# Performance work log

Hardware: AMD Instinct MI355X
Metric: run time of the kernel (lower is better)

The kernel has to match this reference:

```python
import jax, jax.numpy as jnp
import numpy as np

N_NODES, EMB, HID, HEADS, E = 50000, 128, 64, 3, 800000


def setup_inputs() -> dict:
    key = jax.random.key(0)
    ks = jax.random.split(key, 12)
    HC = HEADS * HID
    return {
        "edge_index": jax.random.randint(ks[0], (2, E), 0, N_NODES),
        "edge_attr": jax.random.uniform(ks[1], (E, 1), dtype=jnp.float32),
        "path_emb": jax.random.normal(ks[2], (N_NODES, EMB), dtype=jnp.float32) * (2.0 / EMB) ** 0.5,
        "sim_w": jnp.ones((1,), dtype=jnp.float32),
        "Wl": jax.random.normal(ks[3], (HC, EMB), dtype=jnp.float32) / np.sqrt(EMB),
        "bl": jnp.zeros((HC,), dtype=jnp.float32),
        "Wr": jax.random.normal(ks[4], (HC, EMB), dtype=jnp.float32) / np.sqrt(EMB),
        "br": jnp.zeros((HC,), dtype=jnp.float32),
        "We": jax.random.normal(ks[5], (HC, 1), dtype=jnp.float32),
        "att": jax.random.normal(ks[6], (1, HEADS, HID), dtype=jnp.float32) / np.sqrt(HID),
        "bias_gnn": jnp.zeros((HID,), dtype=jnp.float32),
        "Wout": jax.random.normal(ks[7], (1, HID), dtype=jnp.float32) / np.sqrt(HID),
        "bout": jnp.zeros((1,), dtype=jnp.float32),
    }


def reference(edge_index, edge_attr, path_emb, sim_w, Wl, bl, Wr, br, We, att, bias_gnn, Wout, bout):
    # SimFusionModule: softmax-weighted combination over sim channels -> [E, 1]
    w = jax.nn.softmax(sim_w, axis=0)
    fused = (edge_attr * w).sum(axis=1, keepdims=True)  # [E,1]

    # GATv2Conv (concat=False, no self loops, edge_dim=1)
    xl = (path_emb @ Wl.T + bl).reshape(-1, HEADS, HID)  # source transform [N,H,C]
    xr = (path_emb @ Wr.T + br).reshape(-1, HEADS, HID)  # target transform [N,H,C]
    src, dst = edge_index[0], edge_index[1]
    xj = xl[src]                                          # [E,H,C] gathered source
    xi = xr[dst]                                          # [E,H,C] gathered target
    ef = (fused @ We.T).reshape(-1, HEADS, HID)           # [E,H,C] edge features
    m = xj + xi + ef
    a = (jax.nn.leaky_relu(m, 0.2) * att).sum(-1)         # [E,H] attention logits

    # segment softmax over incoming edges of each destination node
    amax = jax.ops.segment_max(a, dst, num_segments=N_NODES)
    aexp = jnp.exp(a - amax[dst])
    asum = jax.ops.segment_sum(aexp, dst, num_segments=N_NODES)
    alpha = aexp / asum[dst]                              # [E,H]

    out = jax.ops.segment_sum(alpha[:, :, None] * xj, dst, num_segments=N_NODES)  # [N,H,C]
    out = out.mean(axis=1) + bias_gnn                     # concat=False -> head mean, + bias

    scores = (out @ Wout.T + bout).squeeze()              # [N]
    return jax.nn.softmax(scores, axis=0)
```

## Files before the change

### kernel.cpp

```cpp
#include <hip/hip_runtime.h>
#include <cfloat>
#include <cmath>

#define NHEADS 3
#define HIDC   64
#define HCC    192
#define EMBC   128
#define WCOLS  384
#define CAP    1280
#define SCH    4096

typedef unsigned short bhalf;
typedef __fp16 half_t;
typedef __attribute__((ext_vector_type(2))) __fp16 h2;
typedef __attribute__((ext_vector_type(8))) short bf16x8;
typedef __attribute__((ext_vector_type(4))) float f32x4;

__device__ __forceinline__ unsigned f2bf(float f) {
  unsigned u = __float_as_uint(f);
  return (u + 0x7FFFu + ((u >> 16) & 1u)) >> 16;
}
__device__ __forceinline__ unsigned h2bits(h2 v) {
  union { h2 h; unsigned u; } cv; cv.h = v; return cv.u;
}

__global__ __launch_bounds__(256) void prep_kernel(
    const float* __restrict__ Wl, const float* __restrict__ Wr,
    const float* __restrict__ bl, const float* __restrict__ br,
    const float* __restrict__ Wout, const float* __restrict__ We,
    const float* __restrict__ att,
    bhalf* __restrict__ Wb, float* __restrict__ vh, float* __restrict__ bfl,
    unsigned* __restrict__ weh, unsigned* __restrict__ atth,
    float* __restrict__ ch, unsigned* __restrict__ cur,
    float* __restrict__ sumexp, int NB)
{
  const int BASE = WCOLS * EMBC;
  int gt = blockIdx.x * 256 + threadIdx.x;
  if (gt < BASE) {
    int c = gt >> 7, k = gt & 127;
    float v = (c < HCC) ? Wl[c * EMBC + k] : Wr[(c - HCC) * EMBC + k];
    Wb[gt] = (bhalf)f2bf(v);
  } else if (gt < BASE + 384) {
    int i = gt - BASE;
    int h = i >> 7, k = i & 127;
    float s = 0.f;
    for (int c = 0; c < HIDC; ++c)
      s += Wout[c] * Wl[(h * HIDC + c) * EMBC + k];
    vh[i] = s;
  } else if (gt < BASE + 768) {
    int c = gt - BASE - 384;
    bfl[c] = (c < HCC) ? bl[c] : br[c - HCC];
  } else if (gt < BASE + 864) {
    int i = gt - BASE - 768;
    weh[i] = h2bits(__builtin_amdgcn_cvt_pkrtz(We[2 * i], We[2 * i + 1]));
  } else if (gt < BASE + 960) {
    int i = gt - BASE - 864;
    atth[i] = h2bits(__builtin_amdgcn_cvt_pkrtz(att[2 * i], att[2 * i + 1]));
  } else if (gt < BASE + 963) {
    int h = gt - BASE - 960;
    float s = 0.f;
    for (int c = 0; c < HIDC; ++c) s += bl[h * HIDC + c] * Wout[c];
    ch[h] = s;
  } else if (gt < BASE + 963 + NB) {
    int b = gt - BASE - 963;
    cur[b * 16] = (unsigned)(b * CAP);
  } else if (gt == BASE + 963 + NB) {
    *sumexp = 0.f;
  }
}

__global__ __launch_bounds__(256, 4) void gemmscatter_kernel(
    const float* __restrict__ pe, const bhalf* __restrict__ Wb,
    const float* __restrict__ bfl, const float* __restrict__ vh,
    const float* __restrict__ ch,
    half_t* __restrict__ xlh, half_t* __restrict__ xrh,
    float* __restrict__ pj, int N,
    const int* __restrict__ ei, const float* __restrict__ ea,
    uint2* __restrict__ eb, unsigned* __restrict__ cur, int E, int NB2)
{
  __shared__ union {
    bhalf Ws[192 * 64];
    struct { unsigned lh[800]; unsigned lbase[800]; } s;
  } sm;
  const int tid = threadIdx.x;

  if ((int)blockIdx.x < NB2) {
    const int w    = tid >> 6;
    const int lane = tid & 63;
    const int m    = lane & 15;
    const int q    = lane >> 4;
    const int nb   = blockIdx.x >> 1;
    const int half = blockIdx.x & 1;
    const int node = nb * 64 + w * 16 + m;
    const size_t prow = (size_t)(node < N ? node : N - 1) * EMBC;

    bf16x8 pfrag[4];
    float pjp[3] = {0.f, 0.f, 0.f};
    #pragma unroll
    for (int kt = 0; kt < 4; ++kt) {
      const float* p = pe + prow + kt * 32 + q * 8;
      float4 x = *(const float4*)p;
      float4 y = *(const float4*)(p + 4);
      if (half == 0) {
        #pragma unroll
        for (int h = 0; h < 3; ++h) {
          const float* v = vh + h * EMBC + kt * 32 + q * 8;
          float4 va = *(const float4*)v;
          float4 vb = *(const float4*)(v + 4);
          pjp[h] += x.x*va.x + x.y*va.y + x.z*va.z + x.w*va.w
                  + y.x*vb.x + y.y*vb.y + y.z*vb.z + y.w*vb.w;
        }
      }
      union { bf16x8 v; unsigned u[4]; } uu;
      uu.u[0] = (__float_as_uint(x.x) >> 16) | (__float_as_uint(x.y) & 0xFFFF0000u);
      uu.u[1] = (__float_as_uint(x.z) >> 16) | (__float_as_uint(x.w) & 0xFFFF0000u);
      uu.u[2] = (__float_as_uint(y.x) >> 16) | (__float_as_uint(y.y) & 0xFFFF0000u);
      uu.u[3] = (__float_as_uint(y.z) >> 16) | (__float_as_uint(y.w) & 0xFFFF0000u);
      pfrag[kt] = uu.v;
    }

    f32x4 acc[12];
    #pragma unroll
    for (int t = 0; t < 12; ++t) acc[t] = (f32x4){0.f, 0.f, 0.f, 0.f};

    for (int kh = 0; kh < 2; ++kh) {
      __syncthreads();
      for (int f = tid; f < 192 * 8; f += 256) {
        int cc = f >> 3, s = f & 7;
        uint4 v = *(const uint4*)(Wb + (size_t)(half * HCC + cc) * EMBC + kh * 64 + s * 8);
        *(uint4*)(sm.Ws + cc * 64 + ((s ^ (cc & 7)) * 8)) = v;
      }
      __syncthreads();
      #pragma unroll
      for (int kt2 = 0; kt2 < 2; ++kt2) {
        #pragma unroll
        for (int t = 0; t < 12; ++t) {
          bf16x8 wf = *(const bf16x8*)(sm.Ws + (t * 16 + m) * 64 + (((kt2 << 2) + q) ^ (m & 7)) * 8);
          acc[t] = __builtin_amdgcn_mfma_f32_16x16x32_bf16(wf, pfrag[kh * 2 + kt2], acc[t], 0, 0, 0);
        }
      }
    }

    if (half == 0) {
      #pragma unroll
      for (int h = 0; h < 3; ++h) {
        pjp[h] += __shfl_xor(pjp[h], 16);
        pjp[h] += __shfl_xor(pjp[h], 32);
      }
      if (q == 0 && node < N) {
        pj[node * 3 + 0] = pjp[0] + ch[0];
        pj[node * 3 + 1] = pjp[1] + ch[1];
        pj[node * 3 + 2] = pjp[2] + ch[2];
      }
    }

    if (node < N) {
      half_t* xo = half ? xrh : xlh;
      #pragma unroll
      for (int t = 0; t < 12; ++t) {
        int col = t * 16 + q * 4;
        float4 b = *(const float4*)(bfl + half * HCC + col);
        h2 pa = __builtin_amdgcn_cvt_pkrtz(acc[t][0] + b.x, acc[t][1] + b.y);
        h2 pb = __builtin_amdgcn_cvt_pkrtz(acc[t][2] + b.z, acc[t][3] + b.w);
        uint2 st; st.x = h2bits(pa); st.y = h2bits(pb);
        *(uint2*)(xo + (size_t)node * HCC + col) = st;
      }
    }
  } else {
    const int base = (blockIdx.x - NB2) * SCH;
    for (int i = tid; i < 800; i += 256) sm.s.lh[i] = 0;
    __syncthreads();
    #pragma unroll 4
    for (int i = 0; i < SCH / 256; ++i) {
      int e = base + i * 256 + tid;
      if (e < E) atomicAdd(&sm.s.lh[ei[E + e] >> 6], 1u);
    }
    __syncthreads();
    for (int i = tid; i < 800; i += 256) {
      unsigned c = sm.s.lh[i];
      sm.s.lbase[i] = c ? atomicAdd(&cur[i * 16], c) : 0u;
      sm.s.lh[i] = 0;
    }
    __syncthreads();
    #pragma unroll 4
    for (int i = 0; i < SCH / 256; ++i) {
      int e = base + i * 256 + tid;
      if (e < E) {
        int src = ei[e], dst = ei[E + e];
        int bin = dst >> 6;
        unsigned slot = sm.s.lbase[bin] + atomicAdd(&sm.s.lh[bin], 1u);
        uint2 rec;
        rec.x = (unsigned)src | ((unsigned)dst << 16);
        rec.y = __float_as_uint(ea[e]);
        eb[slot] = rec;
      }
    }
  }
}

#define EPG 5
#define GPW 4
#define WCHUNK (EPG * GPW)
__global__ __launch_bounds__(512, 4) void edge_kernel(
    const uint2* __restrict__ eb,
    const half_t* __restrict__ xlh, const half_t* __restrict__ xrh,
    const float* __restrict__ pj, const unsigned* __restrict__ weh,
    const unsigned* __restrict__ atth, const unsigned* __restrict__ cur,
    float* __restrict__ sumexp, float* __restrict__ out, int N)
{
  __shared__ uint4 xrs[64][25];
  __shared__ float facc[64][8];
  const int tid  = threadIdx.x;
  const int w    = tid >> 6;
  const int lane = tid & 63;
  const int j = lane / 12;
  const int c = lane % 12;
  const bool act = lane < 60;
  const int b = blockIdx.x;
  const int n0 = b << 6;
  const int start = b * CAP;
  const int end   = (int)cur[b * 16];

  for (int i = tid; i < 64 * 24; i += 512) {
    int row = i / 24, sl = i % 24;
    int nn = n0 + row; if (nn >= N) nn = N - 1;
    xrs[row][sl] = *(const uint4*)(xrh + (size_t)nn * HCC + sl * 8);
  }
  if (tid < 512) ((float*)facc)[tid] = 0.f;

  union U8 { uint4 u[2]; h2 h[8]; };
  U8 we, at;
  we.u[0] = *(const uint4*)(weh + c * 8);
  we.u[1] = *(const uint4*)(weh + c * 8 + 4);
  at.u[0] = *(const uint4*)(atth + c * 8);
  at.u[1] = *(const uint4*)(atth + c * 8 + 4);
  const h2 c02 = {(__fp16)0.2f, (__fp16)0.2f};
  __syncthreads();

  const int wstart = start + w * WCHUNK;
  uint2 rec[GPW];
  #pragma unroll
  for (int g = 0; g < GPW; ++g) {
    int e = wstart + g * EPG + j;
    rec[g] = eb[e < end ? e : start];
  }

  for (int cb = wstart; cb < end; cb += 8 * WCHUNK) {
    int srcs[GPW], dsts[GPW]; float eavs[GPW];
    #pragma unroll
    for (int g = 0; g < GPW; ++g) {
      srcs[g] = (int)(rec[g].x & 0xFFFFu);
      dsts[g] = (int)(rec[g].x >> 16);
      eavs[g] = __uint_as_float(rec[g].y);
    }
    union U8x { uint4 u[2]; h2 h[8]; };
    U8x ul[GPW]; float pjv[GPW];
    #pragma unroll
    for (int g = 0; g < GPW; ++g) {
      const half_t* rp = xlh + (size_t)srcs[g] * HCC + c * 16;
      ul[g].u[0] = ((const uint4*)rp)[0];
      ul[g].u[1] = ((const uint4*)rp)[1];
    }
    #pragma unroll
    for (int g = 0; g < GPW; ++g)
      pjv[g] = pj[srcs[g] * 3 + (c >> 2)];

    int nxt = cb + 8 * WCHUNK;
    #pragma unroll
    for (int g = 0; g < GPW; ++g) {
      int e = nxt + g * EPG + j;
      rec[g] = eb[(e < end) ? e : start];
    }

    #pragma unroll
    for (int g = 0; g < GPW; ++g) {
      int ld = dsts[g] & 63;
      U8x ur;
      ur.u[0] = xrs[ld][c * 2];
      ur.u[1] = xrs[ld][c * 2 + 1];
      h2 eav2 = __builtin_amdgcn_cvt_pkrtz(eavs[g], eavs[g]);
      float sc = 0.f;
      #pragma unroll
      for (int i = 0; i < 8; ++i) {
        h2 m  = ul[g].h[i] + ur.h[i] + eav2 * we.h[i];
        h2 lr = __builtin_elementwise_max(m, m * c02);
        sc = __builtin_amdgcn_fdot2(lr, at.h[i], sc, false);
      }
      sc += __shfl_xor(sc, 1);
      sc += __shfl_xor(sc, 2);
      bool ve = act && (cb + g * EPG + j < end);
      if (ve && (c & 3) == 0) {
        int h = c >> 2;
        float ex = __expf(sc);
        atomicAdd(&facc[ld][h], ex);
        atomicAdd(&facc[ld][3 + h], ex * pjv[g]);
      }
    }
  }
  __syncthreads();

  if (tid < 64) {
    int n = n0 + tid;
    float e = 0.f;
    if (n < N) {
      float accs = 0.f;
      #pragma unroll
      for (int h = 0; h < 3; ++h) {
        float d = facc[tid][h];
        if (d > 0.f) accs += facc[tid][3 + h] / d;
      }
      e = expf(accs * (1.f / 3.f));
      out[n] = e;
    }
    #pragma unroll
    for (int o = 32; o; o >>= 1) e += __shfl_xor(e, o);
    if (tid == 0) atomicAdd(sumexp, e);
  }
}

__global__ __launch_bounds__(256) void norm_kernel(
    float* __restrict__ out, const float* __restrict__ sumexp, int N)
{
  int n = blockIdx.x * 256 + threadIdx.x;
  if (n < N) out[n] /= *sumexp;
}

extern "C" void kernel_launch(void* const* d_in, const int* in_sizes, int n_in,
                              void* d_out, int out_size, void* d_ws, size_t ws_size,
                              hipStream_t stream) {
  const int*   ei   = (const int*)  d_in[0];
  const float* ea   = (const float*)d_in[1];
  const float* pe   = (const float*)d_in[2];
  const float* Wl   = (const float*)d_in[4];
  const float* bl   = (const float*)d_in[5];
  const float* Wr   = (const float*)d_in[6];
  const float* br   = (const float*)d_in[7];
  const float* We   = (const float*)d_in[8];
  const float* att  = (const float*)d_in[9];
  const float* Wout = (const float*)d_in[11];

  const int E = in_sizes[0] / 2;
  const int N = in_sizes[2] / EMBC;
  const int NB = (N + 63) >> 6;
  float* out = (float*)d_out;

  float* ws       = (float*)d_ws;
  float* sumexp   = ws;
  unsigned* cur   = (unsigned*)(ws + 16);
  float* pj       = ws + 16 + (size_t)NB * 16;
  float* vh       = pj + (size_t)3 * N;
  float* bfl      = vh + 384;
  unsigned* weh   = (unsigned*)(bfl + 384);
  unsigned* atth  = weh + 96;
  float* ch       = (float*)(atth + 96);
  bhalf* Wb       = (bhalf*)(ch + 16);
  half_t* xlh     = (half_t*)(Wb + (size_t)WCOLS * EMBC);
  half_t* xrh     = xlh + (size_t)N * HCC;
  uint2* eb       = (uint2*)(xrh + (size_t)N * HCC);

  const int BASE = WCOLS * EMBC;
  const int NB2 = NB * 2;
  const int NSC = (E + SCH - 1) / SCH;
  prep_kernel<<<(BASE + 963 + NB + 1 + 255) / 256, 256, 0, stream>>>(
      Wl, Wr, bl, br, Wout, We, att, Wb, vh, bfl, weh, atth, ch,
      cur, sumexp, NB);
  gemmscatter_kernel<<<NB2 + NSC, 256, 0, stream>>>(
      pe, Wb, bfl, vh, ch, xlh, xrh, pj, N, ei, ea, eb, cur, E, NB2);
  edge_kernel<<<NB, 512, 0, stream>>>(eb, xlh, xrh, pj, weh, atth, cur,
                                      sumexp, out, N);
  norm_kernel<<<(N + 255) / 256, 256, 0, stream>>>(out, sumexp, N);
}
```

Before: 211.9 us.

## Store node features in fp8, split edge buckets across blocks, add finalize kernel

Node projections xl/xr are now stored as scaled fp8 (x16) rather than fp16, which halves the bytes per gathered row in the edge kernel. The per-destination xr is gathered straight from global memory instead of being staged in shared memory. Each bucket is split across two 256-thread blocks that write partial accumulators, and a new finalize kernel combines them. The pj projection is now computed from the GEMM outputs with Wout instead of a precomputed vh dot product, and the scatter blocks are ordered first. fp8 storage lowers precision and adds conversion work, and the extra kernel launch adds overhead.

```diff
diff --git a/kernel.cpp b/kernel.cpp
--- a/kernel.cpp
+++ b/kernel.cpp
@@ -9,12 +9,14 @@
 #define WCOLS  384
 #define CAP    1280
 #define SCH    4096
+#define SPLIT  2
 
 typedef unsigned short bhalf;
 typedef __fp16 half_t;
 typedef __attribute__((ext_vector_type(2))) __fp16 h2;
 typedef __attribute__((ext_vector_type(8))) short bf16x8;
 typedef __attribute__((ext_vector_type(4))) float f32x4;
+typedef __attribute__((ext_vector_type(2))) float f32x2;
 
 __device__ __forceinline__ unsigned f2bf(float f) {
   unsigned u = __float_as_uint(f);
@@ -27,12 +29,10 @@
 __global__ __launch_bounds__(256) void prep_kernel(
     const float* __restrict__ Wl, const float* __restrict__ Wr,
     const float* __restrict__ bl, const float* __restrict__ br,
-    const float* __restrict__ Wout, const float* __restrict__ We,
-    const float* __restrict__ att,
-    bhalf* __restrict__ Wb, float* __restrict__ vh, float* __restrict__ bfl,
+    const float* __restrict__ We, const float* __restrict__ att,
+    bhalf* __restrict__ Wb, float* __restrict__ bfl,
     unsigned* __restrict__ weh, unsigned* __restrict__ atth,
-    float* __restrict__ ch, unsigned* __restrict__ cur,
-    float* __restrict__ sumexp, int NB)
+    unsigned* __restrict__ cur, float* __restrict__ sumexp, int NB)
 {
   const int BASE = WCOLS * EMBC;
   int gt = blockIdx.x * 256 + threadIdx.x;
@@ -41,42 +41,30 @@
     float v = (c < HCC) ? Wl[c * EMBC + k] : Wr[(c - HCC) * EMBC + k];
     Wb[gt] = (bhalf)f2bf(v);
   } else if (gt < BASE + 384) {
-    int i = gt - BASE;
-    int h = i >> 7, k = i & 127;
-    float s = 0.f;
-    for (int c = 0; c < HIDC; ++c)
-      s += Wout[c] * Wl[(h * HIDC + c) * EMBC + k];
-    vh[i] = s;
-  } else if (gt < BASE + 768) {
-    int c = gt - BASE - 384;
+    int c = gt - BASE;
     bfl[c] = (c < HCC) ? bl[c] : br[c - HCC];
-  } else if (gt < BASE + 864) {
-    int i = gt - BASE - 768;
-    weh[i] = h2bits(__builtin_amdgcn_cvt_pkrtz(We[2 * i], We[2 * i + 1]));
-  } else if (gt < BASE + 960) {
-    int i = gt - BASE - 864;
-    atth[i] = h2bits(__builtin_amdgcn_cvt_pkrtz(att[2 * i], att[2 * i + 1]));
-  } else if (gt < BASE + 963) {
-    int h = gt - BASE - 960;
-    float s = 0.f;
-    for (int c = 0; c < HIDC; ++c) s += bl[h * HIDC + c] * Wout[c];
-    ch[h] = s;
-  } else if (gt < BASE + 963 + NB) {
-    int b = gt - BASE - 963;
+  } else if (gt < BASE + 480) {
+    int i = gt - BASE - 384;
+    weh[i] = h2bits(__builtin_amdgcn_cvt_pkrtz(16.f * We[2 * i], 16.f * We[2 * i + 1]));
+  } else if (gt < BASE + 576) {
+    int i = gt - BASE - 480;
+    atth[i] = h2bits(__builtin_amdgcn_cvt_pkrtz(att[2 * i] * (1.f / 16.f),
+                                                att[2 * i + 1] * (1.f / 16.f)));
+  } else if (gt < BASE + 576 + NB) {
+    int b = gt - BASE - 576;
     cur[b * 16] = (unsigned)(b * CAP);
-  } else if (gt == BASE + 963 + NB) {
+  } else if (gt == BASE + 576 + NB) {
     *sumexp = 0.f;
   }
 }
 
 __global__ __launch_bounds__(256, 4) void gemmscatter_kernel(
     const float* __restrict__ pe, const bhalf* __restrict__ Wb,
-    const float* __restrict__ bfl, const float* __restrict__ vh,
-    const float* __restrict__ ch,
-    half_t* __restrict__ xlh, half_t* __restrict__ xrh,
+    const float* __restrict__ bfl, const float* __restrict__ Wout,
+    unsigned char* __restrict__ xl8, unsigned char* __restrict__ xr8,
     float* __restrict__ pj, int N,
     const int* __restrict__ ei, const float* __restrict__ ea,
-    uint2* __restrict__ eb, unsigned* __restrict__ cur, int E, int NB2)
+    uint2* __restrict__ eb, unsigned* __restrict__ cur, int E, int NSC)
 {
   __shared__ union {
     bhalf Ws[192 * 64];
@@ -84,90 +72,8 @@
   } sm;
   const int tid = threadIdx.x;
 
-  if ((int)blockIdx.x < NB2) {
-    const int w    = tid >> 6;
-    const int lane = tid & 63;
-    const int m    = lane & 15;
-    const int q    = lane >> 4;
-    const int nb   = blockIdx.x >> 1;
-    const int half = blockIdx.x & 1;
-    const int node = nb * 64 + w * 16 + m;
-    const size_t prow = (size_t)(node < N ? node : N - 1) * EMBC;
-
-    bf16x8 pfrag[4];
-    float pjp[3] = {0.f, 0.f, 0.f};
-    #pragma unroll
-    for (int kt = 0; kt < 4; ++kt) {
-      const float* p = pe + prow + kt * 32 + q * 8;
-      float4 x = *(const float4*)p;
-      float4 y = *(const float4*)(p + 4);
-      if (half == 0) {
-        #pragma unroll
-        for (int h = 0; h < 3; ++h) {
-          const float* v = vh + h * EMBC + kt * 32 + q * 8;
-          float4 va = *(const float4*)v;
-          float4 vb = *(const float4*)(v + 4);
-          pjp[h] += x.x*va.x + x.y*va.y + x.z*va.z + x.w*va.w
-                  + y.x*vb.x + y.y*vb.y + y.z*vb.z + y.w*vb.w;
-        }
-      }
-      union { bf16x8 v; unsigned u[4]; } uu;
-      uu.u[0] = (__float_as_uint(x.x) >> 16) | (__float_as_uint(x.y) & 0xFFFF0000u);
-      uu.u[1] = (__float_as_uint(x.z) >> 16) | (__float_as_uint(x.w) & 0xFFFF0000u);
-      uu.u[2] = (__float_as_uint(y.x) >> 16) | (__float_as_uint(y.y) & 0xFFFF0000u);
-      uu.u[3] = (__float_as_uint(y.z) >> 16) | (__float_as_uint(y.w) & 0xFFFF0000u);
-      pfrag[kt] = uu.v;
-    }
-
-    f32x4 acc[12];
-    #pragma unroll
-    for (int t = 0; t < 12; ++t) acc[t] = (f32x4){0.f, 0.f, 0.f, 0.f};
-
-    for (int kh = 0; kh < 2; ++kh) {
-      __syncthreads();
-      for (int f = tid; f < 192 * 8; f += 256) {
-        int cc = f >> 3, s = f & 7;
-        uint4 v = *(const uint4*)(Wb + (size_t)(half * HCC + cc) * EMBC + kh * 64 + s * 8);
-        *(uint4*)(sm.Ws + cc * 64 + ((s ^ (cc & 7)) * 8)) = v;
-      }
-      __syncthreads();
-      #pragma unroll
-      for (int kt2 = 0; kt2 < 2; ++kt2) {
-        #pragma unroll
-        for (int t = 0; t < 12; ++t) {
-          bf16x8 wf = *(const bf16x8*)(sm.Ws + (t * 16 + m) * 64 + (((kt2 << 2) + q) ^ (m & 7)) * 8);
-          acc[t] = __builtin_amdgcn_mfma_f32_16x16x32_bf16(wf, pfrag[kh * 2 + kt2], acc[t], 0, 0, 0);
-        }
-      }
-    }
-
-    if (half == 0) {
-      #pragma unroll
-      for (int h = 0; h < 3; ++h) {
-        pjp[h] += __shfl_xor(pjp[h], 16);
-        pjp[h] += __shfl_xor(pjp[h], 32);
-      }
-      if (q == 0 && node < N) {
-        pj[node * 3 + 0] = pjp[0] + ch[0];
-        pj[node * 3 + 1] = pjp[1] + ch[1];
-        pj[node * 3 + 2] = pjp[2] + ch[2];
-      }
-    }
-
-    if (node < N) {
-      half_t* xo = half ? xrh : xlh;
-      #pragma unroll
-      for (int t = 0; t < 12; ++t) {
-        int col = t * 16 + q * 4;
-        float4 b = *(const float4*)(bfl + half * HCC + col);
-        h2 pa = __builtin_amdgcn_cvt_pkrtz(acc[t][0] + b.x, acc[t][1] + b.y);
-        h2 pb = __builtin_amdgcn_cvt_pkrtz(acc[t][2] + b.z, acc[t][3] + b.w);
-        uint2 st; st.x = h2bits(pa); st.y = h2bits(pb);
-        *(uint2*)(xo + (size_t)node * HCC + col) = st;
-      }
-    }
-  } else {
-    const int base = (blockIdx.x - NB2) * SCH;
+  if ((int)blockIdx.x < NSC) {
+    const int base = blockIdx.x * SCH;
     for (int i = tid; i < 800; i += 256) sm.s.lh[i] = 0;
     __syncthreads();
     #pragma unroll 4
@@ -195,20 +101,103 @@
         eb[slot] = rec;
       }
     }
+  } else {
+    const int bid  = blockIdx.x - NSC;
+    const int w    = tid >> 6;
+    const int lane = tid & 63;
+    const int m    = lane & 15;
+    const int q    = lane >> 4;
+    const int nb   = bid >> 1;
+    const int half = bid & 1;
+    const int node = nb * 64 + w * 16 + m;
+    const size_t prow = (size_t)(node < N ? node : N - 1) * EMBC;
+
+    bf16x8 pfrag[4];
+    #pragma unroll
+    for (int kt = 0; kt < 4; ++kt) {
+      const float* p = pe + prow + kt * 32 + q * 8;
+      float4 x = *(const float4*)p;
+      float4 y = *(const float4*)(p + 4);
+      union { bf16x8 v; unsigned u[4]; } uu;
+      uu.u[0] = (__float_as_uint(x.x) >> 16) | (__float_as_uint(x.y) & 0xFFFF0000u);
+      uu.u[1] = (__float_as_uint(x.z) >> 16) | (__float_as_uint(x.w) & 0xFFFF0000u);
+      uu.u[2] = (__float_as_uint(y.x) >> 16) | (__float_as_uint(y.y) & 0xFFFF0000u);
+      uu.u[3] = (__float_as_uint(y.z) >> 16) | (__float_as_uint(y.w) & 0xFFFF0000u);
+      pfrag[kt] = uu.v;
+    }
+
+    f32x4 acc[12];
+    #pragma unroll
+    for (int t = 0; t < 12; ++t) acc[t] = (f32x4){0.f, 0.f, 0.f, 0.f};
+
+    for (int kh = 0; kh < 2; ++kh) {
+      __syncthreads();
+      for (int f = tid; f < 192 * 8; f += 256) {
+        int cc = f >> 3, s = f & 7;
+        uint4 v = *(const uint4*)(Wb + (size_t)(half * HCC + cc) * EMBC + kh * 64 + s * 8);
+        *(uint4*)(sm.Ws + cc * 64 + ((s ^ (cc & 7)) * 8)) = v;
+      }
+      __syncthreads();
+      #pragma unroll
+      for (int kt2 = 0; kt2 < 2; ++kt2) {
+        #pragma unroll
+        for (int t = 0; t < 12; ++t) {
+          bf16x8 wf = *(const bf16x8*)(sm.Ws + (t * 16 + m) * 64 + (((kt2 << 2) + q) ^ (m & 7)) * 8);
+          acc[t] = __builtin_amdgcn_mfma_f32_16x16x32_bf16(wf, pfrag[kh * 2 + kt2], acc[t], 0, 0, 0);
+        }
+      }
+    }
+
+    float4 wo4[4];
+    #pragma unroll
+    for (int tt = 0; tt < 4; ++tt)
+      wo4[tt] = *(const float4*)(Wout + tt * 16 + q * 4);
+    float pjp[3] = {0.f, 0.f, 0.f};
+    unsigned char* xo = half ? xr8 : xl8;
+    #pragma unroll
+    for (int t = 0; t < 12; ++t) {
+      int col = t * 16 + q * 4;
+      float4 b = *(const float4*)(bfl + half * HCC + col);
+      float r0 = acc[t][0] + b.x;
+      float r1 = acc[t][1] + b.y;
+      float r2 = acc[t][2] + b.z;
+      float r3 = acc[t][3] + b.w;
+      if (half == 0) {
+        float4 wo = wo4[t & 3];
+        pjp[t >> 2] += r0 * wo.x + r1 * wo.y + r2 * wo.z + r3 * wo.w;
+      }
+      if (node < N) {
+        int p = 0;
+        p = __builtin_amdgcn_cvt_pk_fp8_f32(16.f * r0, 16.f * r1, p, false);
+        p = __builtin_amdgcn_cvt_pk_fp8_f32(16.f * r2, 16.f * r3, p, true);
+        *(unsigned*)(xo + (size_t)node * HCC + col) = (unsigned)p;
+      }
+    }
+    if (half == 0) {
+      #pragma unroll
+      for (int h = 0; h < 3; ++h) {
+        pjp[h] += __shfl_xor(pjp[h], 16);
+        pjp[h] += __shfl_xor(pjp[h], 32);
+      }
+      if (q == 0 && node < N) {
+        pj[node * 3 + 0] = pjp[0];
+        pj[node * 3 + 1] = pjp[1];
+        pj[node * 3 + 2] = pjp[2];
+      }
+    }
   }
 }
 
 #define EPG 5
 #define GPW 4
 #define WCHUNK (EPG * GPW)
-__global__ __launch_bounds__(512, 4) void edge_kernel(
+__global__ __launch_bounds__(256, 4) void edge_kernel(
     const uint2* __restrict__ eb,
-    const half_t* __restrict__ xlh, const half_t* __restrict__ xrh,
+    const unsigned char* __restrict__ xl8, const unsigned char* __restrict__ xr8,
     const float* __restrict__ pj, const unsigned* __restrict__ weh,
     const unsigned* __restrict__ atth, const unsigned* __restrict__ cur,
-    float* __restrict__ sumexp, float* __restrict__ out, int N)
-{
-  __shared__ uint4 xrs[64][25];
+    float* __restrict__ pfacc, int N)
+{
   __shared__ float facc[64][8];
   const int tid  = threadIdx.x;
   const int w    = tid >> 6;
@@ -216,28 +205,26 @@
   const int j = lane / 12;
   const int c = lane % 12;
   const bool act = lane < 60;
-  const int b = blockIdx.x;
-  const int n0 = b << 6;
-  const int start = b * CAP;
-  const int end   = (int)cur[b * 16];
-
-  for (int i = tid; i < 64 * 24; i += 512) {
-    int row = i / 24, sl = i % 24;
-    int nn = n0 + row; if (nn >= N) nn = N - 1;
-    xrs[row][sl] = *(const uint4*)(xrh + (size_t)nn * HCC + sl * 8);
-  }
-  if (tid < 512) ((float*)facc)[tid] = 0.f;
+  const int cc = act ? c : 0;
+  const int blk    = blockIdx.x;
+  const int bucket = blk >> 1;
+  const int sl     = blk & 1;
+  const int start = bucket * CAP;
+  const int end   = (int)cur[bucket * 16];
+
+  for (int i = tid; i < 512; i += 256) ((float*)facc)[i] = 0.f;
 
   union U8 { uint4 u[2]; h2 h[8]; };
   U8 we, at;
-  we.u[0] = *(const uint4*)(weh + c * 8);
-  we.u[1] = *(const uint4*)(weh + c * 8 + 4);
-  at.u[0] = *(const uint4*)(atth + c * 8);
-  at.u[1] = *(const uint4*)(atth + c * 8 + 4);
+  we.u[0] = *(const uint4*)(weh + cc * 8);
+  we.u[1] = *(const uint4*)(weh + cc * 8 + 4);
+  at.u[0] = *(const uint4*)(atth + cc * 8);
+  at.u[1] = *(const uint4*)(atth + cc * 8 + 4);
   const h2 c02 = {(__fp16)0.2f, (__fp16)0.2f};
   __syncthreads();
 
-  const int wstart = start + w * WCHUNK;
+  const int gw = sl * 4 + w;
+  const int wstart = start + gw * WCHUNK;
   uint2 rec[GPW];
   #pragma unroll
   for (int g = 0; g < GPW; ++g) {
@@ -253,14 +240,13 @@
       dsts[g] = (int)(rec[g].x >> 16);
       eavs[g] = __uint_as_float(rec[g].y);
     }
-    union U8x { uint4 u[2]; h2 h[8]; };
-    U8x ul[GPW]; float pjv[GPW];
-    #pragma unroll
-    for (int g = 0; g < GPW; ++g) {
-      const half_t* rp = xlh + (size_t)srcs[g] * HCC + c * 16;
-      ul[g].u[0] = ((const uint4*)rp)[0];
-      ul[g].u[1] = ((const uint4*)rp)[1];
-    }
+    uint4 ul[GPW], ur[GPW]; float pjv[GPW];
+    #pragma unroll
+    for (int g = 0; g < GPW; ++g)
+      ul[g] = *(const uint4*)(xl8 + (size_t)srcs[g] * HCC + cc * 16);
+    #pragma unroll
+    for (int g = 0; g < GPW; ++g)
+      ur[g] = *(const uint4*)(xr8 + (size_t)dsts[g] * HCC + cc * 16);
     #pragma unroll
     for (int g = 0; g < GPW; ++g)
       pjv[g] = pj[srcs[g] * 3 + (c >> 2)];
@@ -274,23 +260,33 @@
 
     #pragma unroll
     for (int g = 0; g < GPW; ++g) {
-      int ld = dsts[g] & 63;
-      U8x ur;
-      ur.u[0] = xrs[ld][c * 2];
-      ur.u[1] = xrs[ld][c * 2 + 1];
+      const unsigned* ulp = &ul[g].x;
+      const unsigned* urp = &ur[g].x;
       h2 eav2 = __builtin_amdgcn_cvt_pkrtz(eavs[g], eavs[g]);
       float sc = 0.f;
       #pragma unroll
-      for (int i = 0; i < 8; ++i) {
-        h2 m  = ul[g].h[i] + ur.h[i] + eav2 * we.h[i];
-        h2 lr = __builtin_elementwise_max(m, m * c02);
-        sc = __builtin_amdgcn_fdot2(lr, at.h[i], sc, false);
+      for (int i = 0; i < 4; ++i) {
+        f32x2 la = __builtin_amdgcn_cvt_pk_f32_fp8(ulp[i], false);
+        f32x2 lb = __builtin_amdgcn_cvt_pk_f32_fp8(ulp[i], true);
+        f32x2 ra = __builtin_amdgcn_cvt_pk_f32_fp8(urp[i], false);
+        f32x2 rb = __builtin_amdgcn_cvt_pk_f32_fp8(urp[i], true);
+        h2 l0 = __builtin_amdgcn_cvt_pkrtz(la.x, la.y);
+        h2 l1 = __builtin_amdgcn_cvt_pkrtz(lb.x, lb.y);
+        h2 r0 = __builtin_amdgcn_cvt_pkrtz(ra.x, ra.y);
+        h2 r1 = __builtin_amdgcn_cvt_pkrtz(rb.x, rb.y);
+        h2 m0 = l0 + r0 + eav2 * we.h[2 * i];
+        h2 m1 = l1 + r1 + eav2 * we.h[2 * i + 1];
+        h2 q0 = __builtin_elementwise_max(m0, m0 * c02);
+        h2 q1 = __builtin_elementwise_max(m1, m1 * c02);
+        sc = __builtin_amdgcn_fdot2(q0, at.h[2 * i], sc, false);
+        sc = __builtin_amdgcn_fdot2(q1, at.h[2 * i + 1], sc, false);
       }
       sc += __shfl_xor(sc, 1);
       sc += __shfl_xor(sc, 2);
       bool ve = act && (cb + g * EPG + j < end);
       if (ve && (c & 3) == 0) {
         int h = c >> 2;
+        int ld = dsts[g] & 63;
         float ex = __expf(sc);
         atomicAdd(&facc[ld][h], ex);
         atomicAdd(&facc[ld][3 + h], ex * pjv[g]);
@@ -299,23 +295,41 @@
   }
   __syncthreads();
 
-  if (tid < 64) {
-    int n = n0 + tid;
-    float e = 0.f;
-    if (n < N) {
-      float accs = 0.f;
-      #pragma unroll
-      for (int h = 0; h < 3; ++h) {
-        float d = facc[tid][h];
-        if (d > 0.f) accs += facc[tid][3 + h] / d;
-      }
-      e = expf(accs * (1.f / 3.f));
-      out[n] = e;
-    }
-    #pragma unroll
-    for (int o = 32; o; o >>= 1) e += __shfl_xor(e, o);
-    if (tid == 0) atomicAdd(sumexp, e);
-  }
+  for (int i = tid; i < 512; i += 256)
+    pfacc[(size_t)blk * 512 + i] = ((float*)facc)[i];
+}
+
+__global__ __launch_bounds__(256) void finalize_kernel(
+    const float* __restrict__ pfacc, float* __restrict__ sumexp,
+    float* __restrict__ out, int N)
+{
+  int n = blockIdx.x * 256 + threadIdx.x;
+  int t = threadIdx.x;
+  float e = 0.f;
+  if (n < N) {
+    int bucket = n >> 6, ld = n & 63;
+    float a0 = 0.f, a1 = 0.f, a2 = 0.f, m0 = 0.f, m1 = 0.f, m2 = 0.f;
+    #pragma unroll
+    for (int s = 0; s < SPLIT; ++s) {
+      const float* p = pfacc + ((size_t)(bucket * SPLIT + s) * 512) + ld * 8;
+      a0 += p[0]; a1 += p[1]; a2 += p[2];
+      m0 += p[3]; m1 += p[4]; m2 += p[5];
+    }
+    float accs = 0.f;
+    if (a0 > 0.f) accs += m0 / a0;
+    if (a1 > 0.f) accs += m1 / a1;
+    if (a2 > 0.f) accs += m2 / a2;
+    e = expf(accs * (1.f / 3.f));
+    out[n] = e;
+  }
+  __shared__ float red[256];
+  red[t] = e;
+  __syncthreads();
+  for (int w = 128; w; w >>= 1) {
+    if (t < w) red[t] += red[t + w];
+    __syncthreads();
+  }
+  if (t == 0) atomicAdd(sumexp, red[0]);
 }
 
 __global__ __launch_bounds__(256) void norm_kernel(
@@ -348,25 +362,23 @@
   float* sumexp   = ws;
   unsigned* cur   = (unsigned*)(ws + 16);
   float* pj       = ws + 16 + (size_t)NB * 16;
-  float* vh       = pj + (size_t)3 * N;
-  float* bfl      = vh + 384;
+  float* bfl      = pj + (size_t)3 * N;
   unsigned* weh   = (unsigned*)(bfl + 384);
   unsigned* atth  = weh + 96;
-  float* ch       = (float*)(atth + 96);
-  bhalf* Wb       = (bhalf*)(ch + 16);
-  half_t* xlh     = (half_t*)(Wb + (size_t)WCOLS * EMBC);
-  half_t* xrh     = xlh + (size_t)N * HCC;
-  uint2* eb       = (uint2*)(xrh + (size_t)N * HCC);
+  bhalf* Wb       = (bhalf*)(atth + 96);
+  unsigned char* xl8 = (unsigned char*)(Wb + (size_t)WCOLS * EMBC);
+  unsigned char* xr8 = xl8 + (size_t)N * HCC;
+  uint2* eb       = (uint2*)(xr8 + (size_t)N * HCC);
+  float* pfacc    = (float*)(eb + (size_t)NB * CAP);
 
   const int BASE = WCOLS * EMBC;
-  const int NB2 = NB * 2;
   const int NSC = (E + SCH - 1) / SCH;
-  prep_kernel<<<(BASE + 963 + NB + 1 + 255) / 256, 256, 0, stream>>>(
-      Wl, Wr, bl, br, Wout, We, att, Wb, vh, bfl, weh, atth, ch,
-      cur, sumexp, NB);
-  gemmscatter_kernel<<<NB2 + NSC, 256, 0, stream>>>(
-      pe, Wb, bfl, vh, ch, xlh, xrh, pj, N, ei, ea, eb, cur, E, NB2);
-  edge_kernel<<<NB, 512, 0, stream>>>(eb, xlh, xrh, pj, weh, atth, cur,
-                                      sumexp, out, N);
+  prep_kernel<<<(BASE + 576 + NB + 1 + 255) / 256, 256, 0, stream>>>(
+      Wl, Wr, bl, br, We, att, Wb, bfl, weh, atth, cur, sumexp, NB);
+  gemmscatter_kernel<<<NSC + NB * 2, 256, 0, stream>>>(
+      pe, Wb, bfl, Wout, xl8, xr8, pj, N, ei, ea, eb, cur, E, NSC);
+  edge_kernel<<<NB * SPLIT, 256, 0, stream>>>(eb, xl8, xr8, pj, weh, atth,
+                                              cur, pfacc, N);
+  finalize_kernel<<<(N + 255) / 256, 256, 0, stream>>>(pfacc, sumexp, out, N);
   norm_kernel<<<(N + 255) / 256, 256, 0, stream>>>(out, sumexp, N);
 }
```

After: 190.7 us. 1.11x faster.
